# Performance work log

Measured on AMD Instinct MI355X. Metric: run time of the kernel, lower is better.

Reference implementation:

```python
import jax, jax.numpy as jnp
import numpy as np

A_MIN = 0.001
EPS = 1e-08


def setup_inputs() -> dict:
    key = jax.random.key(0)
    k1, k2, k3, k4 = jax.random.split(key, 4)
    B, O, I = 512, 1024, 512
    x = jax.random.normal(k1, (B, I), dtype=jnp.float32)
    translation = jax.random.uniform(k2, (O, I), dtype=jnp.float32, minval=-1.0, maxval=1.0)
    scale_raw = jax.random.uniform(k3, (O, I), dtype=jnp.float32, minval=-2.0, maxval=0.0)
    weights = jax.random.normal(k4, (O, I), dtype=jnp.float32) * (1.0 / np.sqrt(I))
    return {"x": x, "translation": translation, "scale_raw": scale_raw, "weights": weights}


def reference(x, translation, scale_raw, weights):
    # x: (B, I); params: (O, I)
    scale = A_MIN + jax.nn.softplus(scale_raw)  # (O, I)
    # s: (B, O, I) broadcast intermediate
    s = (x[:, None, :] - translation[None, :, :]) / (scale[None, :, :] + EPS)
    s2 = s * s
    wavelet = (1.0 - s2) * jnp.exp(-0.5 * s2)  # mexican hat
    y = jnp.einsum('oi,boi->bo', weights, wavelet)  # reduce over in_features
    return y
```

## Files before the change

kernel.cpp:

```cpp
#include <hip/hip_runtime.h>


#define WL_A_MIN 0.001f
#define WL_EPS   1e-8f

constexpr int WL_B = 512;
constexpr int WL_O = 1024;
constexpr int WL_I = 512;

#define WL_SQK  0.84932180553704583800f
#define WL_IK   1.38629436111989061883f
#define WL_L2E  1.44269504088896340736f
#define WL_LN2  0.69314718055994530942f

typedef float v2f __attribute__((ext_vector_type(2)));

struct P3 { float nti, inv, w; };

__device__ __forceinline__ float fast_exp2(float a) {
#if __has_builtin(__builtin_amdgcn_exp2f)
    return __builtin_amdgcn_exp2f(a);
#else
    return exp2f(a);
#endif
}
__device__ __forceinline__ float fast_log2(float a) {
#if __has_builtin(__builtin_amdgcn_logf)
    return __builtin_amdgcn_logf(a);
#else
    return __log2f(a);
#endif
}
__device__ __forceinline__ float fast_rcp(float a) {
#if __has_builtin(__builtin_amdgcn_rcpf)
    return __builtin_amdgcn_rcpf(a);
#else
    return 1.0f / a;
#endif
}

#define WL_STEP(PA, PW, OS, XA, XB)                                            \
  do {                                                                         \
    v2f x01 = {(XA).x, (XA).y}, x23 = {(XA).z, (XA).w};                        \
    v2f x45 = {(XB).x, (XB).y}, x67 = {(XB).z, (XB).w};                        \
    v2f s0_, s1_, s2_, s3_, u0_, u1_, u2_, u3_;                                \
    v2f e0_, e1_, e2_, e3_, t0_, t1_, t2_, t3_;                                \
    asm("v_pk_fma_f32 %0, %1, %2, %2 op_sel:[0,1,0] op_sel_hi:[1,1,0]"         \
        : "=v"(s0_) : "v"(x01), "v"(PA));                                      \
    asm("v_pk_fma_f32 %0, %1, %2, %2 op_sel:[0,1,0] op_sel_hi:[1,1,0]"         \
        : "=v"(s1_) : "v"(x23), "v"(PA));                                      \
    asm("v_pk_fma_f32 %0, %1, %2, %2 op_sel:[0,1,0] op_sel_hi:[1,1,0]"         \
        : "=v"(s2_) : "v"(x45), "v"(PA));                                      \
    asm("v_pk_fma_f32 %0, %1, %2, %2 op_sel:[0,1,0] op_sel_hi:[1,1,0]"         \
        : "=v"(s3_) : "v"(x67), "v"(PA));                                      \
    asm("v_pk_mul_f32 %0, %1, %1" : "=v"(u0_) : "v"(s0_));                     \
    asm("v_pk_mul_f32 %0, %1, %1" : "=v"(u1_) : "v"(s1_));                     \
    asm("v_pk_mul_f32 %0, %1, %1" : "=v"(u2_) : "v"(s2_));                     \
    asm("v_pk_mul_f32 %0, %1, %1" : "=v"(u3_) : "v"(s3_));                     \
    e0_.x = fast_exp2(-u0_.x); e0_.y = fast_exp2(-u0_.y);                      \
    e1_.x = fast_exp2(-u1_.x); e1_.y = fast_exp2(-u1_.y);                      \
    e2_.x = fast_exp2(-u2_.x); e2_.y = fast_exp2(-u2_.y);                      \
    e3_.x = fast_exp2(-u3_.x); e3_.y = fast_exp2(-u3_.y);                      \
    asm("v_pk_fma_f32 %0, %1, %2, %0 op_sel:[" OS ",0,0] op_sel_hi:[" OS ",1,1]" \
        : "+v"(aE0) : "v"(PW), "v"(e0_));                                      \
    asm("v_pk_fma_f32 %0, %1, %2, %0 op_sel:[" OS ",0,0] op_sel_hi:[" OS ",1,1]" \
        : "+v"(aE1) : "v"(PW), "v"(e1_));                                      \
    asm("v_pk_fma_f32 %0, %1, %2, %0 op_sel:[" OS ",0,0] op_sel_hi:[" OS ",1,1]" \
        : "+v"(aE2) : "v"(PW), "v"(e2_));                                      \
    asm("v_pk_fma_f32 %0, %1, %2, %0 op_sel:[" OS ",0,0] op_sel_hi:[" OS ",1,1]" \
        : "+v"(aE3) : "v"(PW), "v"(e3_));                                      \
    asm("v_pk_mul_f32 %0, %1, %2" : "=v"(t0_) : "v"(u0_), "v"(e0_));           \
    asm("v_pk_mul_f32 %0, %1, %2" : "=v"(t1_) : "v"(u1_), "v"(e1_));           \
    asm("v_pk_mul_f32 %0, %1, %2" : "=v"(t2_) : "v"(u2_), "v"(e2_));           \
    asm("v_pk_mul_f32 %0, %1, %2" : "=v"(t3_) : "v"(u3_), "v"(e3_));           \
    asm("v_pk_fma_f32 %0, %1, %2, %0 op_sel:[" OS ",0,0] op_sel_hi:[" OS ",1,1]" \
        : "+v"(aU0) : "v"(PW), "v"(t0_));                                      \
    asm("v_pk_fma_f32 %0, %1, %2, %0 op_sel:[" OS ",0,0] op_sel_hi:[" OS ",1,1]" \
        : "+v"(aU1) : "v"(PW), "v"(t1_));                                      \
    asm("v_pk_fma_f32 %0, %1, %2, %0 op_sel:[" OS ",0,0] op_sel_hi:[" OS ",1,1]" \
        : "+v"(aU2) : "v"(PW), "v"(t2_));                                      \
    asm("v_pk_fma_f32 %0, %1, %2, %0 op_sel:[" OS ",0,0] op_sel_hi:[" OS ",1,1]" \
        : "+v"(aU3) : "v"(PW), "v"(t3_));                                      \
  } while (0)

__global__ __launch_bounds__(256) void wl_prep(
    const float* __restrict__ translation,
    const float* __restrict__ scale_raw,
    const float* __restrict__ weights,
    v2f* __restrict__ A2,
    v2f* __restrict__ W2)
{
    __shared__ P3 lds[16 * 64];
    const int t  = threadIdx.x;
    const int o0 = blockIdx.x * 64;
    const int i0 = blockIdx.y * 16;

    {
        const int o_l = t >> 2;
        const int iq  = t & 3;
        const size_t g = (size_t)(o0 + o_l) * WL_I + (i0 + iq * 4);
        const float4 tv = *reinterpret_cast<const float4*>(translation + g);
        const float4 sv = *reinterpret_cast<const float4*>(scale_raw   + g);
        const float4 wv = *reinterpret_cast<const float4*>(weights     + g);
        const float tt[4] = {tv.x, tv.y, tv.z, tv.w};
        const float ss[4] = {sv.x, sv.y, sv.z, sv.w};
        const float ww[4] = {wv.x, wv.y, wv.z, wv.w};
        #pragma unroll
        for (int j = 0; j < 4; ++j) {
            float ex  = fast_exp2(ss[j] * WL_L2E);
            float sp  = fast_log2(1.0f + ex) * WL_LN2;
            float inv = fast_rcp(WL_A_MIN + sp + WL_EPS) * WL_SQK;
            P3 pv; pv.nti = -tt[j] * inv; pv.inv = inv; pv.w = ww[j];
            lds[(iq * 4 + j) * 64 + o_l] = pv;
        }
    }
    __syncthreads();
    {
        const int o_l = t & 63;
        const int r   = t >> 6;
        const int o   = o0 + o_l;
        #pragma unroll
        for (int jp = 0; jp < 2; ++jp) {
            const int i_l = r * 4 + jp * 2;
            P3 a = lds[i_l * 64 + o_l];
            P3 b = lds[(i_l + 1) * 64 + o_l];
            A2[(size_t)(i0 + i_l)     * WL_O + o] = (v2f){a.nti, a.inv};
            A2[(size_t)(i0 + i_l + 1) * WL_O + o] = (v2f){b.nti, b.inv};
            W2[(size_t)((i0 + i_l) >> 1) * WL_O + o] = (v2f){a.w, b.w};
        }
    }
}

__global__ __launch_bounds__(512, 6) void wl_main(
    const float* __restrict__ x,
    const v2f* __restrict__ A2,
    const v2f* __restrict__ W2,
    float* __restrict__ out)
{
    __shared__ float smem[16 * 513];

    const int tid  = threadIdx.x;
    const int lane = tid & 63;
    const int wid  = tid >> 6;
    const int o    = blockIdx.x * 64 + lane;
    const int b0   = blockIdx.y * 8;

    {
        const int b_l = tid & 7;
        const int seg = tid >> 3;
        const float* xg = &x[(size_t)(b0 + b_l) * WL_I + seg * 8];
        const float4 v0 = *reinterpret_cast<const float4*>(xg);
        const float4 v1 = *reinterpret_cast<const float4*>(xg + 4);
        const int base = seg * 64 + b_l;
        smem[base +  0] = v0.x;
        smem[base +  8] = v0.y;
        smem[base + 16] = v0.z;
        smem[base + 24] = v0.w;
        smem[base + 32] = v1.x;
        smem[base + 40] = v1.y;
        smem[base + 48] = v1.z;
        smem[base + 56] = v1.w;
    }
    __syncthreads();

    const v2f* __restrict__ pA = A2 + (size_t)(wid * 64) * WL_O + o;
    const v2f* __restrict__ pW = W2 + (size_t)(wid * 32) * WL_O + o;
    const float* xr = &smem[wid * 64 * 8];

    v2f aE0 = {0.f,0.f}, aE1 = {0.f,0.f}, aE2 = {0.f,0.f}, aE3 = {0.f,0.f};
    v2f aU0 = {0.f,0.f}, aU1 = {0.f,0.f}, aU2 = {0.f,0.f}, aU3 = {0.f,0.f};

    #pragma unroll 2
    for (int g = 0; g < 32; ++g) {
        const v2f pa0 = pA[0];
        const v2f pa1 = pA[WL_O];
        const v2f pw  = pW[0];
        pA += 2 * WL_O;  pW += WL_O;
        const float4 xa0 = ((const float4*)xr)[0];
        const float4 xb0 = ((const float4*)xr)[1];
        const float4 xa1 = ((const float4*)xr)[2];
        const float4 xb1 = ((const float4*)xr)[3];
        xr += 16;
        WL_STEP(pa0, pw, "0", xa0, xb0);
        WL_STEP(pa1, pw, "1", xa1, xb1);
    }

    __syncthreads();
    {
        const int c = wid * 64 + lane;
        const float vals[16] = {aE0.x,aE0.y,aE1.x,aE1.y,aE2.x,aE2.y,aE3.x,aE3.y,
                                aU0.x,aU0.y,aU1.x,aU1.y,aU2.x,aU2.y,aU3.x,aU3.y};
        #pragma unroll
        for (int k = 0; k < 16; ++k)
            smem[k * 513 + c] = vals[k];
    }
    __syncthreads();
    {
        float E = 0.f, U = 0.f;
        #pragma unroll
        for (int sw = 0; sw < 8; ++sw) {
            E += smem[wid * 513       + sw * 64 + lane];
            U += smem[(8 + wid) * 513 + sw * 64 + lane];
        }
        out[(size_t)(b0 + wid) * WL_O + o] = fmaf(-WL_IK, U, E);
    }
}

extern "C" void kernel_launch(void* const* d_in, const int* in_sizes, int n_in,
                              void* d_out, int out_size, void* d_ws, size_t ws_size,
                              hipStream_t stream) {
    const float* x           = (const float*)d_in[0];
    const float* translation = (const float*)d_in[1];
    const float* scale_raw   = (const float*)d_in[2];
    const float* weights     = (const float*)d_in[3];
    float*       out         = (float*)d_out;
    v2f* A2 = (v2f*)d_ws;
    v2f* W2 = (v2f*)((char*)d_ws + (size_t)WL_I * WL_O * sizeof(v2f));

    wl_prep<<<dim3(WL_O / 64, WL_I / 16), dim3(256), 0, stream>>>(
        translation, scale_raw, weights, A2, W2);

    wl_main<<<dim3(WL_O / 64, WL_B / 8), dim3(512), 0, stream>>>(
        x, A2, W2, out);
}
```

Baseline: 110.2 us.

## Fold mexican-hat polynomial into weights to merge E and U accumulators

Instead of accumulating w·e and w·u·e separately and combining at the end, each step forms v = w − k·w·u with one packed FMA and then accumulates v·e into a single accumulator set. This removes the separate multiply and the second accumulator chain, cutting packed VALU ops per step and halving accumulator registers. The weight workspace becomes one float per input index instead of packed pairs, and launch bounds are raised to allow more waves per CU. It adds a scalar multiply per iteration and narrower weight loads, and the occupancy hint could cause spilling if registers tighten.

```diff
diff --git a/kernel.cpp b/kernel.cpp
--- a/kernel.cpp
+++ b/kernel.cpp
@@ -39,12 +39,12 @@
 #endif
 }
 
-#define WL_STEP(PA, PW, OS, XA, XB)                                            \
+#define WL_STEP(PA, PW, XA, XB)                                                \
   do {                                                                         \
     v2f x01 = {(XA).x, (XA).y}, x23 = {(XA).z, (XA).w};                        \
     v2f x45 = {(XB).x, (XB).y}, x67 = {(XB).z, (XB).w};                        \
     v2f s0_, s1_, s2_, s3_, u0_, u1_, u2_, u3_;                                \
-    v2f e0_, e1_, e2_, e3_, t0_, t1_, t2_, t3_;                                \
+    v2f e0_, e1_, e2_, e3_, v0_, v1_, v2_, v3_;                                \
     asm("v_pk_fma_f32 %0, %1, %2, %2 op_sel:[0,1,0] op_sel_hi:[1,1,0]"         \
         : "=v"(s0_) : "v"(x01), "v"(PA));                                      \
     asm("v_pk_fma_f32 %0, %1, %2, %2 op_sel:[0,1,0] op_sel_hi:[1,1,0]"         \
@@ -61,26 +61,18 @@
     e1_.x = fast_exp2(-u1_.x); e1_.y = fast_exp2(-u1_.y);                      \
     e2_.x = fast_exp2(-u2_.x); e2_.y = fast_exp2(-u2_.y);                      \
     e3_.x = fast_exp2(-u3_.x); e3_.y = fast_exp2(-u3_.y);                      \
-    asm("v_pk_fma_f32 %0, %1, %2, %0 op_sel:[" OS ",0,0] op_sel_hi:[" OS ",1,1]" \
-        : "+v"(aE0) : "v"(PW), "v"(e0_));                                      \
-    asm("v_pk_fma_f32 %0, %1, %2, %0 op_sel:[" OS ",0,0] op_sel_hi:[" OS ",1,1]" \
-        : "+v"(aE1) : "v"(PW), "v"(e1_));                                      \
-    asm("v_pk_fma_f32 %0, %1, %2, %0 op_sel:[" OS ",0,0] op_sel_hi:[" OS ",1,1]" \
-        : "+v"(aE2) : "v"(PW), "v"(e2_));                                      \
-    asm("v_pk_fma_f32 %0, %1, %2, %0 op_sel:[" OS ",0,0] op_sel_hi:[" OS ",1,1]" \
-        : "+v"(aE3) : "v"(PW), "v"(e3_));                                      \
-    asm("v_pk_mul_f32 %0, %1, %2" : "=v"(t0_) : "v"(u0_), "v"(e0_));           \
-    asm("v_pk_mul_f32 %0, %1, %2" : "=v"(t1_) : "v"(u1_), "v"(e1_));           \
-    asm("v_pk_mul_f32 %0, %1, %2" : "=v"(t2_) : "v"(u2_), "v"(e2_));           \
-    asm("v_pk_mul_f32 %0, %1, %2" : "=v"(t3_) : "v"(u3_), "v"(e3_));           \
-    asm("v_pk_fma_f32 %0, %1, %2, %0 op_sel:[" OS ",0,0] op_sel_hi:[" OS ",1,1]" \
-        : "+v"(aU0) : "v"(PW), "v"(t0_));                                      \
-    asm("v_pk_fma_f32 %0, %1, %2, %0 op_sel:[" OS ",0,0] op_sel_hi:[" OS ",1,1]" \
-        : "+v"(aU1) : "v"(PW), "v"(t1_));                                      \
-    asm("v_pk_fma_f32 %0, %1, %2, %0 op_sel:[" OS ",0,0] op_sel_hi:[" OS ",1,1]" \
-        : "+v"(aU2) : "v"(PW), "v"(t2_));                                      \
-    asm("v_pk_fma_f32 %0, %1, %2, %0 op_sel:[" OS ",0,0] op_sel_hi:[" OS ",1,1]" \
-        : "+v"(aU3) : "v"(PW), "v"(t3_));                                      \
+    asm("v_pk_fma_f32 %0, %1, %2, %1 op_sel:[1,0,0] op_sel_hi:[1,1,0]"         \
+        : "=v"(v0_) : "v"(PW), "v"(u0_));                                      \
+    asm("v_pk_fma_f32 %0, %1, %2, %1 op_sel:[1,0,0] op_sel_hi:[1,1,0]"         \
+        : "=v"(v1_) : "v"(PW), "v"(u1_));                                      \
+    asm("v_pk_fma_f32 %0, %1, %2, %1 op_sel:[1,0,0] op_sel_hi:[1,1,0]"         \
+        : "=v"(v2_) : "v"(PW), "v"(u2_));                                      \
+    asm("v_pk_fma_f32 %0, %1, %2, %1 op_sel:[1,0,0] op_sel_hi:[1,1,0]"         \
+        : "=v"(v3_) : "v"(PW), "v"(u3_));                                      \
+    asm("v_pk_fma_f32 %0, %1, %2, %0" : "+v"(acc0) : "v"(v0_), "v"(e0_));      \
+    asm("v_pk_fma_f32 %0, %1, %2, %0" : "+v"(acc1) : "v"(v1_), "v"(e1_));      \
+    asm("v_pk_fma_f32 %0, %1, %2, %0" : "+v"(acc2) : "v"(v2_), "v"(e2_));      \
+    asm("v_pk_fma_f32 %0, %1, %2, %0" : "+v"(acc3) : "v"(v3_), "v"(e3_));      \
   } while (0)
 
 __global__ __launch_bounds__(256) void wl_prep(
@@ -88,7 +80,7 @@
     const float* __restrict__ scale_raw,
     const float* __restrict__ weights,
     v2f* __restrict__ A2,
-    v2f* __restrict__ W2)
+    float* __restrict__ W1)
 {
     __shared__ P3 lds[16 * 64];
     const int t  = threadIdx.x;
@@ -120,24 +112,22 @@
         const int r   = t >> 6;
         const int o   = o0 + o_l;
         #pragma unroll
-        for (int jp = 0; jp < 2; ++jp) {
-            const int i_l = r * 4 + jp * 2;
+        for (int j = 0; j < 4; ++j) {
+            const int i_l = r * 4 + j;
             P3 a = lds[i_l * 64 + o_l];
-            P3 b = lds[(i_l + 1) * 64 + o_l];
-            A2[(size_t)(i0 + i_l)     * WL_O + o] = (v2f){a.nti, a.inv};
-            A2[(size_t)(i0 + i_l + 1) * WL_O + o] = (v2f){b.nti, b.inv};
-            W2[(size_t)((i0 + i_l) >> 1) * WL_O + o] = (v2f){a.w, b.w};
+            A2[(size_t)(i0 + i_l) * WL_O + o] = (v2f){a.nti, a.inv};
+            W1[(size_t)(i0 + i_l) * WL_O + o] = a.w;
         }
     }
 }
 
-__global__ __launch_bounds__(512, 6) void wl_main(
+__global__ __launch_bounds__(512, 8) void wl_main(
     const float* __restrict__ x,
     const v2f* __restrict__ A2,
-    const v2f* __restrict__ W2,
+    const float* __restrict__ W1,
     float* __restrict__ out)
 {
-    __shared__ float smem[16 * 513];
+    __shared__ float smem[8 * 513];
 
     const int tid  = threadIdx.x;
     const int lane = tid & 63;
@@ -163,46 +153,40 @@
     }
     __syncthreads();
 
-    const v2f* __restrict__ pA = A2 + (size_t)(wid * 64) * WL_O + o;
-    const v2f* __restrict__ pW = W2 + (size_t)(wid * 32) * WL_O + o;
+    const v2f*   __restrict__ pA = A2 + (size_t)(wid * 64) * WL_O + o;
+    const float* __restrict__ pW = W1 + (size_t)(wid * 64) * WL_O + o;
     const float* xr = &smem[wid * 64 * 8];
 
-    v2f aE0 = {0.f,0.f}, aE1 = {0.f,0.f}, aE2 = {0.f,0.f}, aE3 = {0.f,0.f};
-    v2f aU0 = {0.f,0.f}, aU1 = {0.f,0.f}, aU2 = {0.f,0.f}, aU3 = {0.f,0.f};
-
-    #pragma unroll 2
-    for (int g = 0; g < 32; ++g) {
-        const v2f pa0 = pA[0];
-        const v2f pa1 = pA[WL_O];
-        const v2f pw  = pW[0];
-        pA += 2 * WL_O;  pW += WL_O;
-        const float4 xa0 = ((const float4*)xr)[0];
-        const float4 xb0 = ((const float4*)xr)[1];
-        const float4 xa1 = ((const float4*)xr)[2];
-        const float4 xb1 = ((const float4*)xr)[3];
-        xr += 16;
-        WL_STEP(pa0, pw, "0", xa0, xb0);
-        WL_STEP(pa1, pw, "1", xa1, xb1);
+    v2f acc0 = {0.f,0.f}, acc1 = {0.f,0.f}, acc2 = {0.f,0.f}, acc3 = {0.f,0.f};
+
+    #pragma unroll 4
+    for (int ii = 0; ii < 64; ++ii) {
+        const v2f   pa = *pA;  pA += WL_O;
+        v2f pw;
+        pw.x = *pW;  pW += WL_O;
+        pw.y = pw.x * (-WL_IK);
+        const float4 xa = ((const float4*)xr)[0];
+        const float4 xb = ((const float4*)xr)[1];
+        xr += 8;
+        WL_STEP(pa, pw, xa, xb);
     }
 
     __syncthreads();
     {
         const int c = wid * 64 + lane;
-        const float vals[16] = {aE0.x,aE0.y,aE1.x,aE1.y,aE2.x,aE2.y,aE3.x,aE3.y,
-                                aU0.x,aU0.y,aU1.x,aU1.y,aU2.x,aU2.y,aU3.x,aU3.y};
-        #pragma unroll
-        for (int k = 0; k < 16; ++k)
+        const float vals[8] = {acc0.x, acc0.y, acc1.x, acc1.y,
+                               acc2.x, acc2.y, acc3.x, acc3.y};
+        #pragma unroll
+        for (int k = 0; k < 8; ++k)
             smem[k * 513 + c] = vals[k];
     }
     __syncthreads();
     {
-        float E = 0.f, U = 0.f;
-        #pragma unroll
-        for (int sw = 0; sw < 8; ++sw) {
-            E += smem[wid * 513       + sw * 64 + lane];
-            U += smem[(8 + wid) * 513 + sw * 64 + lane];
-        }
-        out[(size_t)(b0 + wid) * WL_O + o] = fmaf(-WL_IK, U, E);
+        float y = 0.f;
+        #pragma unroll
+        for (int sw = 0; sw < 8; ++sw)
+            y += smem[wid * 513 + sw * 64 + lane];
+        out[(size_t)(b0 + wid) * WL_O + o] = y;
     }
 }
 
@@ -214,12 +198,12 @@
     const float* scale_raw   = (const float*)d_in[2];
     const float* weights     = (const float*)d_in[3];
     float*       out         = (float*)d_out;
-    v2f* A2 = (v2f*)d_ws;
-    v2f* W2 = (v2f*)((char*)d_ws + (size_t)WL_I * WL_O * sizeof(v2f));
+    v2f*   A2 = (v2f*)d_ws;
+    float* W1 = (float*)((char*)d_ws + (size_t)WL_I * WL_O * sizeof(v2f));
 
     wl_prep<<<dim3(WL_O / 64, WL_I / 16), dim3(256), 0, stream>>>(
-        translation, scale_raw, weights, A2, W2);
+        translation, scale_raw, weights, A2, W1);
 
     wl_main<<<dim3(WL_O / 64, WL_B / 8), dim3(512), 0, stream>>>(
-        x, A2, W2, out);
-}
+        x, A2, W1, out);
+}
```

Result: faster. 107.1 us (-2.8%).
